# Kernel tuning notes

Hardware: AMD Instinct MI355X
Metric: run time of the kernel (lower is better)

Reference implementation:

```python
import jax, jax.numpy as jnp
import numpy as np

B, L, N = 16, 512, 32          # batch, seq_length, feature_size
E = 128                        # embed_size == frequency_size (number_frequency=1)
EMB = 8                        # embedding_dim
FCH = 64                       # fc_hidden_dim
H = 256                        # hidden_size
PRE = 96                       # pre_length
LAMBDA = 0.01                  # sparsity_threshold
SCALE = 0.02                   # init_scale


def softshrink(v, lambd=LAMBDA):
    return jnp.where(v > lambd, v - lambd, jnp.where(v < -lambd, v + lambd, 0.0))


def setup_inputs() -> dict:
    key = jax.random.key(0)
    ks = jax.random.split(key, 16)
    f32 = jnp.float32
    return {
        "x": jax.random.normal(ks[0], (B, L, N), f32),
        "emb": jax.random.normal(ks[1], (1, E), f32),
        "w0": SCALE * jax.random.normal(ks[2], (2, E, E), f32),
        "b0": SCALE * jax.random.normal(ks[3], (2, E), f32),
        "w1": SCALE * jax.random.normal(ks[4], (2, E, E), f32),
        "b1": SCALE * jax.random.normal(ks[5], (2, E), f32),
        "w2": SCALE * jax.random.normal(ks[6], (2, E, E), f32),
        "b2": SCALE * jax.random.normal(ks[7], (2, E), f32),
        "emb10": jax.random.normal(ks[8], (L, EMB), f32),
        "fc1_w": jax.random.normal(ks[9], (FCH, E * EMB), f32) / np.sqrt(E * EMB),
        "fc1_b": jnp.zeros((FCH,), f32),
        "fc2_w": jax.random.normal(ks[10], (H, FCH), f32) / np.sqrt(FCH),
        "fc2_b": jnp.zeros((H,), f32),
        "fc3_w": jax.random.normal(ks[11], (PRE, H), f32) / np.sqrt(H),
        "fc3_b": jnp.zeros((PRE,), f32),
    }


def _diag(w):
    # einsum 'bli,ii->bli' multiplies by the DIAGONAL of w only
    return jnp.diagonal(w, axis1=-2, axis2=-1)


def reference(x, emb, w0, b0, w1, b1, w2, b2, emb10,
              fc1_w, fc1_b, fc2_w, fc2_b, fc3_w, fc3_b):
    Bb = x.shape[0]
    xt = jnp.transpose(x, (0, 2, 1)).reshape(Bb, -1)          # [B, N*L]
    tok = xt[:, :, None] * emb                                 # [B, N*L, E]
    xf = jnp.fft.rfft(tok, axis=1, norm="ortho")               # [B, N*L//2+1, E] complex
    bias = xf

    # --- fourierGC (faithful to the torch op ordering, incl. o_real reuse) ---
    relu = jax.nn.relu
    d00, d01 = _diag(w0[0]), _diag(w0[1])
    o_r = relu(xf.real * d00 - xf.imag * d01 + b0[0])
    o_i = relu(xf.imag * d00 + xf.real * d01 + b0[1])
    prev = softshrink(jnp.stack([o_r, o_i], axis=-1))

    # middle layer (num_layers=3 -> one): note o_i uses the UPDATED o_r, as in torch
    d10, d11 = _diag(w1[0]), _diag(w1[1])
    o_r_new = relu(o_r * d10 - o_i * d11 + b1[0])
    o_i = relu(o_i * d10 + o_r_new * d11 + b1[1])
    o_r = o_r_new
    prev = softshrink(jnp.stack([o_r, o_i], axis=-1)) + prev

    # last layer
    d20, d21 = _diag(w2[0]), _diag(w2[1])
    o_r_new = relu(o_r * d20 - o_i * d21 + b2[0])
    o_i = relu(o_i * d20 + o_r_new * d21 + b2[1])
    z = softshrink(jnp.stack([o_r_new, o_i], axis=-1)) + prev
    zc = jax.lax.complex(z[..., 0], z[..., 1])

    xf = zc + bias
    xt = jnp.fft.irfft(xf, n=N * L, axis=1, norm="ortho")      # [B, N*L, E]
    xt = xt.reshape(Bb, N, L, E)
    xt = jnp.transpose(xt, (0, 1, 3, 2))                        # [B, N, E, L]
    h = jnp.matmul(xt, emb10)                                   # [B, N, E, EMB]
    h = h.reshape(Bb, N, E * EMB)

    lrelu = lambda v: jax.nn.leaky_relu(v, 0.01)
    h = lrelu(h @ fc1_w.T + fc1_b)
    h = lrelu(h @ fc2_w.T + fc2_b)
    out = h @ fc3_w.T + fc3_b                                   # [B, N, PRE]
    return out[:, 0, :]                                         # target_idx = 0
```

## Files before the change

kernel.cpp:

```cpp
#include <hip/hip_runtime.h>
#include <math.h>

#define Bsz   16
#define Lseq  512
#define Nfeat 32
#define E     128
#define EMB   8
#define FCH   64
#define Hd    256
#define PRE   96
#define M     16384
#define MH    8193
#define LAMBDA 0.01f

#define OFF_G   0
#define OFF_CS  524288
#define OFF_P   655376

#define REV_M   6.103515625e-5f
#define REV_128 7.8125e-3f

__device__ __forceinline__ float sin_rev(float r) { return __builtin_amdgcn_sinf(r); }
__device__ __forceinline__ float cos_rev(float r) { return __builtin_amdgcn_cosf(r); }

__global__ __launch_bounds__(256, 4)
void k_prep(const float* __restrict__ x, const float* __restrict__ emb10,
            float* __restrict__ ws) {
  __shared__ __align__(16) float sbuf[4160];
  int bid = blockIdx.x, tid = threadIdx.x;
  {
    int b = bid >> 6, t1base = (bid & 63) << 1;
    int t1loc = tid >> 7, idx = tid & 127;
    {
      int t = (t1base + t1loc) + 128 * idx;
      int n = t >> 9, l = t & 511;
      sbuf[t1loc * 128 + idx] = x[b * (Lseq * Nfeat) + l * Nfeat + n];
    }
    __syncthreads();
    int f1 = idx, t1 = t1base + t1loc;
    float s1 = sin_rev((float)f1 * REV_128), c1 = cos_rev((float)f1 * REV_128);
    float c2 = c1 * c1 - s1 * s1, s2 = 2.f * s1 * c1;
    float cA = 1.f, sA = 0.f, cB = c1, sB = s1;
    float grA = 0.f, giA = 0.f, grB = 0.f, giB = 0.f;
    const float2* xc2 = (const float2*)(sbuf + t1loc * 128);
    #pragma unroll 8
    for (int h = 0; h < 64; ++h) {
      float2 xv = xc2[h];
      grA = fmaf(xv.x, cA, grA); giA = fmaf(xv.x, -sA, giA);
      grB = fmaf(xv.y, cB, grB); giB = fmaf(xv.y, -sB, giB);
      float cn = cA * c2 - sA * s2; sA = sA * c2 + cA * s2; cA = cn;
      cn = cB * c2 - sB * s2;       sB = sB * c2 + cB * s2; cB = cn;
    }
    float gr = grA + grB, gi = giA + giB;
    float rv = (float)(f1 * t1) * REV_M;
    float sb = sin_rev(rv), cb = cos_rev(rv);
    float grr = gr * cb + gi * sb;
    float gii = gi * cb - gr * sb;
    float* G = ws + OFF_G + ((b * 128 + f1) * 128 + t1) * 2;
    G[0] = grr; G[1] = gii;
  }
  __syncthreads();
  {
    for (int j = tid; j < Lseq * EMB; j += 256) {
      int t = j >> 3, m = j & 7;
      sbuf[m * 512 + t] = emb10[j];
    }
    __syncthreads();
    int floc = tid >> 5, tl = tid & 31;
    int f = bid * 8 + floc;
    float ca[EMB], sa[EMB];
    #pragma unroll
    for (int m = 0; m < EMB; ++m) { ca[m] = 0.f; sa[m] = 0.f; }
    #pragma unroll 4
    for (int it = 0; it < 16; ++it) {
      int t = tl + 32 * it;
      int k = (f * t) & (M - 1);
      float rv = (float)k * REV_M;
      float cc = cos_rev(rv), ss = sin_rev(rv);
      #pragma unroll
      for (int m = 0; m < EMB; ++m) {
        float ev = sbuf[m * 512 + t];
        ca[m] = fmaf(cc, ev, ca[m]);
        sa[m] = fmaf(ss, ev, sa[m]);
      }
    }
    #pragma unroll
    for (int off = 16; off >= 1; off >>= 1) {
      #pragma unroll
      for (int m = 0; m < EMB; ++m) {
        ca[m] += __shfl_xor(ca[m], off, 64);
        sa[m] += __shfl_xor(sa[m], off, 64);
      }
    }
    if (tl == 0) {
      float wf = (f == 0) ? (1.0f / 128.0f) : (2.0f / 128.0f);
      float* o = ws + OFF_CS + f * 16;
      #pragma unroll
      for (int m = 0; m < EMB; ++m) { o[m] = ca[m] * wf; o[8 + m] = sa[m] * wf; }
    }
    if (bid == 0 && tid < 64) {
      int m = tid & 7, g = tid >> 3;
      float p = 0.f;
      #pragma unroll 8
      for (int j = 0; j < 64; ++j) p += sbuf[m * 512 + g + 8 * j];
      p = (g & 1) ? -p : p;
      p += __shfl_xor(p, 8, 64);
      p += __shfl_xor(p, 16, 64);
      p += __shfl_xor(p, 32, 64);
      if (g == 0) {
        ws[OFF_CS + 8192 * 16 + m] = p * (1.0f / 128.0f);
        ws[OFF_CS + 8192 * 16 + 8 + m] = 0.f;
      }
    }
  }
}

__global__ __launch_bounds__(1024, 8)
void k_gcf(const float* __restrict__ emb,
           const float* __restrict__ w0, const float* __restrict__ b0,
           const float* __restrict__ w1, const float* __restrict__ b1,
           const float* __restrict__ w2, const float* __restrict__ b2,
           float* __restrict__ ws) {
  __shared__ __align__(16) float2 Gs[4 * 132];
  __shared__ __align__(16) float2 Xs[257];
  __shared__ float red[7 * 1024];
  int f1g = blockIdx.x, b = blockIdx.y, tid = threadIdx.x;
  int f1base = f1g * 4;
  if (tid < 512) {
    float2 v = ((const float2*)(ws + OFF_G + (b * 128 + f1base) * 256))[tid];
    int f1loc = tid >> 7, t1 = tid & 127;
    Gs[f1loc * 132 + (t1 >> 5) * 33 + (t1 & 31)] = v;
  }
  __syncthreads();
  {
    int w = tid >> 6, lane = tid & 63;
    int f1loc = w >> 2;
    int q = lane >> 4, f2 = ((w & 3) << 4) + (lane & 15);
    int r = (f2 * q) & 3;
    float c = (r == 0) ? 1.f : (r == 2) ? -1.f : 0.f;
    float s = (r == 1) ? 1.f : (r == 3) ? -1.f : 0.f;
    float s1 = sin_rev((float)f2 * REV_128), c1 = cos_rev((float)f2 * REV_128);
    float xr = 0.f, xi = 0.f;
    const float2* g = Gs + f1loc * 132 + q * 33;
    #pragma unroll 8
    for (int k = 0; k < 32; ++k) {
      float2 gv = g[k];
      xr = fmaf(gv.x, c, xr); xr = fmaf(gv.y, s, xr);
      xi = fmaf(gv.y, c, xi); xi = fmaf(-gv.x, s, xi);
      float cn = c * c1 - s * s1; s = s * c1 + c * s1; c = cn;
    }
    xr += __shfl_xor(xr, 16, 64); xi += __shfl_xor(xi, 16, 64);
    xr += __shfl_xor(xr, 32, 64); xi += __shfl_xor(xi, 32, 64);
    if (lane < 16) Xs[f1loc * 64 + f2] = make_float2(xr, xi);
    if (f1base == 0 && tid < 64) {
      int t1v = tid * 2;
      const float2* g0p = Gs + (t1v >> 5) * 33;
      float2 g0 = g0p[t1v & 31], g1 = g0p[(t1v & 31) + 1];
      float er = g0.x - g1.x, ei = g0.y - g1.y;
      #pragma unroll
      for (int off = 1; off <= 32; off <<= 1) {
        er += __shfl_xor(er, off, 64);
        ei += __shfl_xor(ei, off, 64);
      }
      if (tid == 0) Xs[256] = make_float2(er, ei);
    }
  }
  __syncthreads();
  int e = tid & 127, fh = tid >> 7;
  int nf = (f1base == 0) ? 257 : 256;
  float se  = emb[e] * (1.0f / 128.0f);
  float d00 = w0[e * 129], d01 = w0[E * E + e * 129];
  float c00 = b0[e],       c01 = b0[E + e];
  float d10 = w1[e * 129], d11 = w1[E * E + e * 129];
  float c10 = b1[e],       c11 = b1[E + e];
  float d20 = w2[e * 129], d21 = w2[E * E + e * 129];
  float c20 = b2[e],       c21 = b2[E + e];
  float acc[EMB];
  #pragma unroll
  for (int m = 0; m < EMB; ++m) acc[m] = 0.f;

  for (int i = fh; i < nf; i += 8) {
    int iu = __builtin_amdgcn_readfirstlane(i);
    int f = (iu == 256) ? 8192 : (f1base + (iu >> 6) + ((iu & 63) << 7));
    const float* cs = ws + OFF_CS + f * 16;
    float2 X = Xs[iu];
    float xr = X.x * se, xi = X.y * se;
    float or0 = fmaxf(fmaf(xr, d00, fmaf(-xi, d01, c00)), 0.f);
    float oi0 = fmaxf(fmaf(xi, d00, fmaf(xr, d01, c01)), 0.f);
    float pr = fmaxf(or0 - LAMBDA, 0.f), pi = fmaxf(oi0 - LAMBDA, 0.f);
    float or1 = fmaxf(fmaf(or0, d10, fmaf(-oi0, d11, c10)), 0.f);
    float oi1 = fmaxf(fmaf(oi0, d10, fmaf(or1, d11, c11)), 0.f);
    pr += fmaxf(or1 - LAMBDA, 0.f); pi += fmaxf(oi1 - LAMBDA, 0.f);
    float u2r = fmaf(or1, d20, fmaf(-oi1, d21, c20));
    float or2 = fmaxf(u2r, 0.f);
    float u2i = fmaf(oi1, d20, fmaf(or2, d21, c21));
    float zr = fmaxf(u2r - LAMBDA, 0.f) + pr;
    float zi = fmaxf(u2i - LAMBDA, 0.f) + pi;
    #pragma unroll
    for (int m = 0; m < EMB; ++m)
      acc[m] = fmaf(zr, cs[m], fmaf(-zi, cs[8 + m], acc[m]));
  }
  __syncthreads();
  if (fh > 0) {
    #pragma unroll
    for (int m = 0; m < EMB; ++m) red[(fh - 1) * 1024 + e * EMB + m] = acc[m];
  }
  __syncthreads();
  if (fh == 0) {
    #pragma unroll
    for (int j = 0; j < 7; ++j)
      #pragma unroll
      for (int m = 0; m < EMB; ++m) acc[m] += red[j * 1024 + e * EMB + m];
    float* P = ws + OFF_P + (f1g * 16 + b) * (E * EMB) + e * EMB;
    #pragma unroll
    for (int m = 0; m < EMB; ++m) P[m] = acc[m];
  }
}

__global__ __launch_bounds__(1024)
void k_fc(const float* __restrict__ x, const float* __restrict__ emb,
          const float* __restrict__ emb10,
          const float* __restrict__ fc1w, const float* __restrict__ fc1b,
          const float* __restrict__ fc2w, const float* __restrict__ fc2b,
          const float* __restrict__ fc3w, const float* __restrict__ fc3b,
          const float* __restrict__ ws, float* __restrict__ out) {
  int b = blockIdx.x;
  __shared__ float h0s[E * EMB];
  __shared__ float h1s[FCH];
  __shared__ float h2s[Hd];
  __shared__ float hxs[EMB];
  __shared__ float scratch[1024];
  int tid = threadIdx.x;
  int lane = tid & 63, w = tid >> 6;
  {
    int m = tid & 7, g = tid >> 3;
    float p = 0.f;
    #pragma unroll
    for (int l = g; l < Lseq; l += 128)
      p = fmaf(x[b * (Lseq * Nfeat) + l * Nfeat], emb10[l * EMB + m], p);
    scratch[tid] = p;
  }
  const float* P = ws + OFF_P + b * (E * EMB) + tid;
  float a = 0.f;
  #pragma unroll
  for (int c = 0; c < 32; ++c) a += P[c * (Bsz * E * EMB)];
  __syncthreads();
  if (tid < 8) {
    float s = 0.f;
    #pragma unroll 16
    for (int g = 0; g < 128; ++g) s += scratch[g * 8 + tid];
    hxs[tid] = s;
  }
  __syncthreads();
  h0s[tid] = a + emb[tid >> 3] * hxs[tid & 7];
  __syncthreads();
  #pragma unroll
  for (int oo = 0; oo < 4; ++oo) {
    int o = oo * 16 + w;
    const float* wr = fc1w + o * (E * EMB);
    float acc = 0.f;
    #pragma unroll
    for (int j = 0; j < 16; ++j) acc = fmaf(h0s[lane + 64 * j], wr[lane + 64 * j], acc);
    #pragma unroll
    for (int off = 32; off >= 1; off >>= 1) acc += __shfl_xor(acc, off, 64);
    if (lane == 0) { float v = acc + fc1b[o]; h1s[o] = v > 0.f ? v : 0.01f * v; }
  }
  __syncthreads();
  #pragma unroll
  for (int oo = 0; oo < 16; ++oo) {
    int o = oo * 16 + w;
    float acc = h1s[lane] * fc2w[o * FCH + lane];
    #pragma unroll
    for (int off = 32; off >= 1; off >>= 1) acc += __shfl_xor(acc, off, 64);
    if (lane == 0) { float v = acc + fc2b[o]; h2s[o] = v > 0.f ? v : 0.01f * v; }
  }
  __syncthreads();
  #pragma unroll
  for (int oo = 0; oo < 6; ++oo) {
    int o = oo * 16 + w;
    const float* wr = fc3w + o * Hd;
    float acc = 0.f;
    #pragma unroll
    for (int j = 0; j < 4; ++j) acc = fmaf(h2s[lane + 64 * j], wr[lane + 64 * j], acc);
    #pragma unroll
    for (int off = 32; off >= 1; off >>= 1) acc += __shfl_xor(acc, off, 64);
    if (lane == 0) out[b * PRE + o] = acc + fc3b[o];
  }
}

extern "C" void kernel_launch(void* const* d_in, const int* in_sizes, int n_in,
                              void* d_out, int out_size, void* d_ws, size_t ws_size,
                              hipStream_t stream) {
  const float* x     = (const float*)d_in[0];
  const float* emb   = (const float*)d_in[1];
  const float* w0    = (const float*)d_in[2];
  const float* b0    = (const float*)d_in[3];
  const float* w1    = (const float*)d_in[4];
  const float* b1    = (const float*)d_in[5];
  const float* w2    = (const float*)d_in[6];
  const float* b2    = (const float*)d_in[7];
  const float* emb10 = (const float*)d_in[8];
  const float* fc1w  = (const float*)d_in[9];
  const float* fc1b  = (const float*)d_in[10];
  const float* fc2w  = (const float*)d_in[11];
  const float* fc2b  = (const float*)d_in[12];
  const float* fc3w  = (const float*)d_in[13];
  const float* fc3b  = (const float*)d_in[14];
  float* ws  = (float*)d_ws;
  float* out = (float*)d_out;

  k_prep<<<dim3(1024), 256, 0, stream>>>(x, emb10, ws);
  k_gcf<<<dim3(32, Bsz), 1024, 0, stream>>>(emb, w0, b0, w1, b1, w2, b2, ws);
  k_fc<<<dim3(Bsz), 1024, 0, stream>>>(x, emb, emb10, fc1w, fc1b, fc2w, fc2b,
                                       fc3w, fc3b, ws, out);
}
```

Measured before the change: 148.4 us.

## Fuse first FFT stage into k_gcf and split CS table into separate kernel

The first radix-128 DFT stage (G twiddled partials) is no longer computed in k_prep and written to global workspace. Each k_gcf block now loads its batch's whole x slice into padded shared memory and recomputes the G values for its four f1 rows directly. The remaining prep work (the emb10 cos/sin table) becomes a smaller k_cs kernel with 4x more frequencies per block. This removes the global G round trip, but each batch's x is loaded 32 times and k_gcf uses much more shared memory, which may reduce occupancy.

Result: no change. 151.3 us (+2.0%).

```diff
diff --git a/kernel.cpp b/kernel.cpp
--- a/kernel.cpp
+++ b/kernel.cpp
@@ -13,9 +13,8 @@
 #define MH    8193
 #define LAMBDA 0.01f
 
-#define OFF_G   0
-#define OFF_CS  524288
-#define OFF_P   655376
+#define OFF_CS  0
+#define OFF_P   131088
 
 #define REV_M   6.103515625e-5f
 #define REV_128 7.8125e-3f
@@ -24,50 +23,18 @@
 __device__ __forceinline__ float cos_rev(float r) { return __builtin_amdgcn_cosf(r); }
 
 __global__ __launch_bounds__(256, 4)
-void k_prep(const float* __restrict__ x, const float* __restrict__ emb10,
-            float* __restrict__ ws) {
-  __shared__ __align__(16) float sbuf[4160];
+void k_cs(const float* __restrict__ emb10, float* __restrict__ ws) {
+  __shared__ float e10T[Lseq * EMB];
   int bid = blockIdx.x, tid = threadIdx.x;
-  {
-    int b = bid >> 6, t1base = (bid & 63) << 1;
-    int t1loc = tid >> 7, idx = tid & 127;
-    {
-      int t = (t1base + t1loc) + 128 * idx;
-      int n = t >> 9, l = t & 511;
-      sbuf[t1loc * 128 + idx] = x[b * (Lseq * Nfeat) + l * Nfeat + n];
-    }
-    __syncthreads();
-    int f1 = idx, t1 = t1base + t1loc;
-    float s1 = sin_rev((float)f1 * REV_128), c1 = cos_rev((float)f1 * REV_128);
-    float c2 = c1 * c1 - s1 * s1, s2 = 2.f * s1 * c1;
-    float cA = 1.f, sA = 0.f, cB = c1, sB = s1;
-    float grA = 0.f, giA = 0.f, grB = 0.f, giB = 0.f;
-    const float2* xc2 = (const float2*)(sbuf + t1loc * 128);
-    #pragma unroll 8
-    for (int h = 0; h < 64; ++h) {
-      float2 xv = xc2[h];
-      grA = fmaf(xv.x, cA, grA); giA = fmaf(xv.x, -sA, giA);
-      grB = fmaf(xv.y, cB, grB); giB = fmaf(xv.y, -sB, giB);
-      float cn = cA * c2 - sA * s2; sA = sA * c2 + cA * s2; cA = cn;
-      cn = cB * c2 - sB * s2;       sB = sB * c2 + cB * s2; cB = cn;
-    }
-    float gr = grA + grB, gi = giA + giB;
-    float rv = (float)(f1 * t1) * REV_M;
-    float sb = sin_rev(rv), cb = cos_rev(rv);
-    float grr = gr * cb + gi * sb;
-    float gii = gi * cb - gr * sb;
-    float* G = ws + OFF_G + ((b * 128 + f1) * 128 + t1) * 2;
-    G[0] = grr; G[1] = gii;
-  }
-  __syncthreads();
-  {
-    for (int j = tid; j < Lseq * EMB; j += 256) {
-      int t = j >> 3, m = j & 7;
-      sbuf[m * 512 + t] = emb10[j];
-    }
-    __syncthreads();
-    int floc = tid >> 5, tl = tid & 31;
-    int f = bid * 8 + floc;
+  for (int j = tid; j < Lseq * EMB; j += 256) {
+    int t = j >> 3, m = j & 7;
+    e10T[m * 512 + t] = emb10[j];
+  }
+  __syncthreads();
+  int floc = tid >> 5, tl = tid & 31;
+  #pragma unroll
+  for (int ff = 0; ff < 4; ++ff) {
+    int f = bid * 32 + ff * 8 + floc;
     float ca[EMB], sa[EMB];
     #pragma unroll
     for (int m = 0; m < EMB; ++m) { ca[m] = 0.f; sa[m] = 0.f; }
@@ -79,7 +46,7 @@
       float cc = cos_rev(rv), ss = sin_rev(rv);
       #pragma unroll
       for (int m = 0; m < EMB; ++m) {
-        float ev = sbuf[m * 512 + t];
+        float ev = e10T[m * 512 + t];
         ca[m] = fmaf(cc, ev, ca[m]);
         sa[m] = fmaf(ss, ev, sa[m]);
       }
@@ -98,38 +65,66 @@
       #pragma unroll
       for (int m = 0; m < EMB; ++m) { o[m] = ca[m] * wf; o[8 + m] = sa[m] * wf; }
     }
-    if (bid == 0 && tid < 64) {
-      int m = tid & 7, g = tid >> 3;
-      float p = 0.f;
-      #pragma unroll 8
-      for (int j = 0; j < 64; ++j) p += sbuf[m * 512 + g + 8 * j];
-      p = (g & 1) ? -p : p;
-      p += __shfl_xor(p, 8, 64);
-      p += __shfl_xor(p, 16, 64);
-      p += __shfl_xor(p, 32, 64);
-      if (g == 0) {
-        ws[OFF_CS + 8192 * 16 + m] = p * (1.0f / 128.0f);
-        ws[OFF_CS + 8192 * 16 + 8 + m] = 0.f;
-      }
+  }
+  if (bid == 0 && tid < 64) {
+    int m = tid & 7, g = tid >> 3;
+    float p = 0.f;
+    #pragma unroll 8
+    for (int j = 0; j < 64; ++j) p += e10T[m * 512 + g + 8 * j];
+    p = (g & 1) ? -p : p;
+    p += __shfl_xor(p, 8, 64);
+    p += __shfl_xor(p, 16, 64);
+    p += __shfl_xor(p, 32, 64);
+    if (g == 0) {
+      ws[OFF_CS + 8192 * 16 + m] = p * (1.0f / 128.0f);
+      ws[OFF_CS + 8192 * 16 + 8 + m] = 0.f;
     }
   }
 }
 
+#define XPAD(t) ((t) + ((t) >> 9))
 __global__ __launch_bounds__(1024, 8)
-void k_gcf(const float* __restrict__ emb,
+void k_gcf(const float* __restrict__ x, const float* __restrict__ emb,
            const float* __restrict__ w0, const float* __restrict__ b0,
            const float* __restrict__ w1, const float* __restrict__ b1,
            const float* __restrict__ w2, const float* __restrict__ b2,
            float* __restrict__ ws) {
+  __shared__ __align__(16) float xf[16416];
   __shared__ __align__(16) float2 Gs[4 * 132];
-  __shared__ __align__(16) float2 Xs[257];
-  __shared__ float red[7 * 1024];
+  float2* Xs = (float2*)xf;
+  float* red = xf + 1024;
   int f1g = blockIdx.x, b = blockIdx.y, tid = threadIdx.x;
   int f1base = f1g * 4;
+  {
+    const float* xb = x + b * (Lseq * Nfeat);
+    #pragma unroll
+    for (int i = tid; i < Lseq * Nfeat; i += 1024) {
+      int l = i >> 5, n = i & 31;
+      xf[n * 513 + l] = xb[i];
+    }
+  }
+  __syncthreads();
   if (tid < 512) {
-    float2 v = ((const float2*)(ws + OFF_G + (b * 128 + f1base) * 256))[tid];
     int f1loc = tid >> 7, t1 = tid & 127;
-    Gs[f1loc * 132 + (t1 >> 5) * 33 + (t1 & 31)] = v;
+    int f1 = f1base + f1loc;
+    float s1 = sin_rev((float)f1 * REV_128), c1 = cos_rev((float)f1 * REV_128);
+    float c2 = c1 * c1 - s1 * s1, s2 = 2.f * s1 * c1;
+    float cA = 1.f, sA = 0.f, cB = c1, sB = s1;
+    float grA = 0.f, giA = 0.f, grB = 0.f, giB = 0.f;
+    #pragma unroll 8
+    for (int t2 = 0; t2 < 128; t2 += 2) {
+      int ta = t1 + 128 * t2;
+      float x0 = xf[XPAD(ta)], x1 = xf[XPAD(ta + 128)];
+      grA = fmaf(x0, cA, grA); giA = fmaf(x0, -sA, giA);
+      grB = fmaf(x1, cB, grB); giB = fmaf(x1, -sB, giB);
+      float cn = cA * c2 - sA * s2; sA = sA * c2 + cA * s2; cA = cn;
+      cn = cB * c2 - sB * s2;       sB = sB * c2 + cB * s2; cB = cn;
+    }
+    float gr = grA + grB, gi = giA + giB;
+    float rv = (float)(f1 * t1) * REV_M;
+    float sb = sin_rev(rv), cb = cos_rev(rv);
+    Gs[f1loc * 132 + (t1 >> 5) * 33 + (t1 & 31)] =
+        make_float2(gr * cb + gi * sb, gi * cb - gr * sb);
   }
   __syncthreads();
   {
@@ -309,8 +304,8 @@
   float* ws  = (float*)d_ws;
   float* out = (float*)d_out;
 
-  k_prep<<<dim3(1024), 256, 0, stream>>>(x, emb10, ws);
-  k_gcf<<<dim3(32, Bsz), 1024, 0, stream>>>(emb, w0, b0, w1, b1, w2, b2, ws);
+  k_cs<<<dim3(256), 256, 0, stream>>>(emb10, ws);
+  k_gcf<<<dim3(32, Bsz), 1024, 0, stream>>>(x, emb, w0, b0, w1, b1, w2, b2, ws);
   k_fc<<<dim3(Bsz), 1024, 0, stream>>>(x, emb, emb10, fc1w, fc1b, fc2w, fc2b,
                                        fc3w, fc3b, ws, out);
 }
```
